# Optimization experiments

Hardware: AMD Instinct MI355X
Metric: run time of the kernel (lower is better)

Reference implementation:

```python
import jax, jax.numpy as jnp
import numpy as np

B, H, S, D, KG = 1, 8, 1024, 64, 10

def setup_inputs() -> dict:
    key = jax.random.key(0)
    ks = jax.random.split(key, 16)
    n = jax.random.normal
    u = jax.random.uniform
    return {
        'Q': n(ks[0], (B, H, S, D), dtype=jnp.float32),
        'K': n(ks[1], (B, H, S, D), dtype=jnp.float32),
        'V': n(ks[2], (B, H, S, D), dtype=jnp.float32),
        'distance_matrix': u(ks[3], (B, H, S, S), dtype=jnp.float32) * 10.0,
        'energy_matrix': u(ks[4], (B, H, S, S), dtype=jnp.float32) * 5.0,
        'mask': jnp.ones((B, H, S, S), dtype=jnp.int32),
        'mu_D': n(ks[5], (KG,), dtype=jnp.float32),
        'sigma_D': u(ks[6], (KG,), dtype=jnp.float32) + 0.5,  # keep sigma positive
        'b_D': n(ks[7], (KG,), dtype=jnp.float32) * 0.1,
        'mu_E': n(ks[8], (KG,), dtype=jnp.float32),
        'sigma_E': u(ks[9], (KG,), dtype=jnp.float32) + 0.5,
        'b_E': n(ks[10], (KG,), dtype=jnp.float32) * 0.1,
        'W1': n(ks[11], (KG, KG), dtype=jnp.float32) / np.sqrt(KG),
        'b1': jnp.zeros((KG,), dtype=jnp.float32),
        'W2': n(ks[12], (1, KG), dtype=jnp.float32) / np.sqrt(KG),
        'b2': jnp.zeros((1,), dtype=jnp.float32),
    }


def _rbf_mlp_bias(x, b, mu, sigma, W1, b1, W2, b2):
    # x: [B,H,S,S] -> Gaussian RBF features over K kernels, then small MLP -> [B,H,S,S]
    z = (x[..., None] + b - mu) / sigma                      # [B,H,S,S,K]
    inv_norm = 1.0 / (jnp.sqrt(2.0 * jnp.pi) * sigma)
    psi = jnp.exp(-0.5 * z * z) * inv_norm                   # [B,H,S,S,K]
    h = jax.nn.gelu(jnp.einsum('bhijk,lk->bhijl', psi, W1) + b1, approximate=False)
    return (jnp.einsum('bhijk,lk->bhijl', h, W2) + b2)[..., 0]


def reference(Q, K, V, distance_matrix, energy_matrix, mask,
              mu_D, sigma_D, b_D, mu_E, sigma_E, b_E, W1, b1, W2, b2):
    d_model = Q.shape[-1]
    scores = jnp.einsum('bhid,bhjd->bhij', Q, K) / np.sqrt(d_model * 2)
    scores = scores + _rbf_mlp_bias(distance_matrix, b_D, mu_D, sigma_D, W1, b1, W2, b2)
    scores = scores + _rbf_mlp_bias(energy_matrix, b_E, mu_E, sigma_E, W1, b1, W2, b2)
    scores = jnp.where(mask == 0, jnp.float32(-1e9), scores)
    attn = jax.nn.softmax(scores, axis=-1)
    return jnp.einsum('bhij,bhjd->bhid', attn, V)
```

## Files before the change

kernel.cpp:

```cpp
#include <hip/hip_runtime.h>
#include <math.h>

#define Hn 8
#define Sn 1024
#define Dn 64
#define KG 10

#define TN 2048
#define RD 10.25f
#define RE 5.125f

typedef __attribute__((ext_vector_type(8))) short bf16x8;
typedef __attribute__((ext_vector_type(4))) float f32x4;
typedef unsigned short u16;
typedef unsigned int u32;

__device__ inline float bf2f(u16 u) {
    union { u32 i; float f; } v;
    v.i = ((u32)u) << 16;
    return v.f;
}

__device__ inline u16 f2bf(float f) {
    union { float f; u32 i; } v;
    v.f = f;
    u32 i = v.i;
    return (u16)((i + 0x7FFFu + ((i >> 16) & 1u)) >> 16);
}

__device__ float bias_eval(float x,
                           const float* __restrict__ mu, const float* __restrict__ sg,
                           const float* __restrict__ bb,
                           const float* __restrict__ W1, const float* __restrict__ b1,
                           const float* __restrict__ W2, const float* __restrict__ b2) {
    const float inv_s2pi = 0.39894228040143267794f;
    float psi[KG];
#pragma unroll
    for (int k = 0; k < KG; k++) {
        float s = sg[k];
        float z = (x + bb[k] - mu[k]) / s;
        psi[k] = __expf(-0.5f * z * z) * (inv_s2pi / s);
    }
    float out = b2[0];
#pragma unroll
    for (int l = 0; l < KG; l++) {
        float a = b1[l];
#pragma unroll
        for (int k = 0; k < KG; k++) a += psi[k] * W1[l * KG + k];
        float g = 0.5f * a * (1.0f + erff(a * 0.70710678118654752440f));
        out += g * W2[l];
    }
    return out;
}

#define QK4 262144
#define VTN 524288

__global__ __launch_bounds__(256) void prep_kernel(
    const float* __restrict__ Q, const float* __restrict__ K, const float* __restrict__ V,
    const float* __restrict__ muD, const float* __restrict__ sgD, const float* __restrict__ bD,
    const float* __restrict__ muE, const float* __restrict__ sgE, const float* __restrict__ bE,
    const float* __restrict__ W1, const float* __restrict__ b1,
    const float* __restrict__ W2, const float* __restrict__ b2,
    u32* __restrict__ tab, u16* __restrict__ Qb, u16* __restrict__ Kb, u16* __restrict__ VTi)
{
    int id = blockIdx.x * 256 + threadIdx.x;
    if (id < 2 * TN) {
        int which = (id >= TN);
        int idx = id & (TN - 1);
        float h = (which ? RE : RD) / (float)TN;
        float x0 = idx * h;
        float v0, v1;
        if (which) {
            v0 = bias_eval(x0,     muE, sgE, bE, W1, b1, W2, b2);
            v1 = bias_eval(x0 + h, muE, sgE, bE, W1, b1, W2, b2);
        } else {
            v0 = bias_eval(x0,     muD, sgD, bD, W1, b1, W2, b2);
            v1 = bias_eval(x0 + h, muD, sgD, bD, W1, b1, W2, b2);
        }
        tab[id] = (u32)f2bf(v0) | ((u32)f2bf(v1 - v0) << 16);
    } else if (id < 2 * TN + QK4) {
        int i = id - 2 * TN;
        int arr = i >> 17;
        i &= (1 << 17) - 1;
        float4 v = ((const float4*)(arr ? K : Q))[i];
        ushort4 o;
        o.x = f2bf(v.x); o.y = f2bf(v.y); o.z = f2bf(v.z); o.w = f2bf(v.w);
        ((ushort4*)(arr ? Kb : Qb))[i] = o;
    } else if (id < 2 * TN + QK4 + VTN) {
        int g = id - (2 * TN + QK4);
        int h = g >> 16;
        int d = (g >> 10) & 63;
        int s = g & 1023;
        int t = s >> 5, q = (s >> 3) & 3, j = s & 7;
        int src_s = (t << 5) + (q << 2) + (j & 3) + ((j >> 2) << 4);
        VTi[g] = f2bf(V[(((size_t)h << 10) + src_s) * Dn + d]);
    }
}

__device__ inline float lerp_tab(const u32* __restrict__ st, float x, float invh) {
    float tf = x * invh;
    int i = (int)tf;
    float fr = tf - (float)i;
    u32 p = st[i];
    return fmaf(bf2f((u16)(p >> 16)), fr, bf2f((u16)p));
}

__global__ __launch_bounds__(512, 4) void attn_kernel(
    const u16* __restrict__ Qb, const u16* __restrict__ Kb, const u16* __restrict__ VTi,
    const float* __restrict__ Dm, const float* __restrict__ Em, const int* __restrict__ Mk,
    const u32* __restrict__ gtab, float* __restrict__ out)
{
    __shared__ __align__(16) u32 sTab[2 * TN];
    __shared__ float sO[8][16][68];
    __shared__ float sL[8][16];

    const int tid = threadIdx.x;
    {
        const uint4* g4 = (const uint4*)gtab;
        uint4* s4 = (uint4*)sTab;
        s4[tid] = g4[tid];
        s4[tid + 512] = g4[tid + 512];
    }
    __syncthreads();

    const int h    = blockIdx.y;
    const int q0   = blockIdx.x * 16;
    const int wave = tid >> 6;
    const int lane = tid & 63;
    const int quad = lane >> 4;
    const int l16  = lane & 15;

    const u16* Qh = Qb  + (size_t)h * Sn * Dn;
    const u16* Kh = Kb  + (size_t)h * Sn * Dn;
    const u16* Vh = VTi + (size_t)h * Dn * Sn;
    const float* Dh = Dm + (size_t)h * Sn * Sn + (size_t)(q0 + l16) * Sn;
    const float* Eh = Em + (size_t)h * Sn * Sn + (size_t)(q0 + l16) * Sn;
    const int*   Mh = Mk + (size_t)h * Sn * Sn + (size_t)(q0 + l16) * Sn;
    const float invhD = (float)TN / RD;
    const float invhE = (float)TN / RE;
    const float scale = 0.08838834764831845f;
    const float Mfix  = 16.f;

    const bf16x8 bQ0 = *(const bf16x8*)(Qh + (q0 + l16) * Dn + quad * 8);
    const bf16x8 bQ1 = *(const bf16x8*)(Qh + (q0 + l16) * Dn + 32 + quad * 8);

    f32x4 O0 = {0.f, 0.f, 0.f, 0.f}, O1 = O0, O2 = O0, O3 = O0;
    float l_r = 0.f;

    const int kbase = wave * 128;
#pragma unroll
    for (int t = 0; t < 4; t++) {
        const int k0 = kbase + t * 32;

        const u16* kr = Kh + (size_t)(k0 + l16) * Dn + quad * 8;
        const bf16x8 aK00 = *(const bf16x8*)(kr);
        const bf16x8 aK01 = *(const bf16x8*)(kr + 32);
        const bf16x8 aK10 = *(const bf16x8*)(kr + 16 * Dn);
        const bf16x8 aK11 = *(const bf16x8*)(kr + 16 * Dn + 32);

        const u16* vr = Vh + k0 + quad * 8;
        const bf16x8 bV0 = *(const bf16x8*)(vr + (size_t)(l16)      * Sn);
        const bf16x8 bV1 = *(const bf16x8*)(vr + (size_t)(16 + l16) * Sn);
        const bf16x8 bV2 = *(const bf16x8*)(vr + (size_t)(32 + l16) * Sn);
        const bf16x8 bV3 = *(const bf16x8*)(vr + (size_t)(48 + l16) * Sn);

        const float4 Dv0 = *(const float4*)(Dh + k0 + quad * 4);
        const float4 Dv1 = *(const float4*)(Dh + k0 + 16 + quad * 4);
        const float4 Ev0 = *(const float4*)(Eh + k0 + quad * 4);
        const float4 Ev1 = *(const float4*)(Eh + k0 + 16 + quad * 4);
        const int4   Mv0 = *(const int4*)(Mh + k0 + quad * 4);
        const int4   Mv1 = *(const int4*)(Mh + k0 + 16 + quad * 4);

        f32x4 s0 = {0.f, 0.f, 0.f, 0.f}, s1 = s0;
        s0 = __builtin_amdgcn_mfma_f32_16x16x32_bf16(aK00, bQ0, s0, 0, 0, 0);
        s0 = __builtin_amdgcn_mfma_f32_16x16x32_bf16(aK01, bQ1, s0, 0, 0, 0);
        s1 = __builtin_amdgcn_mfma_f32_16x16x32_bf16(aK10, bQ0, s1, 0, 0, 0);
        s1 = __builtin_amdgcn_mfma_f32_16x16x32_bf16(aK11, bQ1, s1, 0, 0, 0);

        const float dv0[4] = {Dv0.x, Dv0.y, Dv0.z, Dv0.w};
        const float dv1[4] = {Dv1.x, Dv1.y, Dv1.z, Dv1.w};
        const float ev0[4] = {Ev0.x, Ev0.y, Ev0.z, Ev0.w};
        const float ev1[4] = {Ev1.x, Ev1.y, Ev1.z, Ev1.w};
        const int   mv0[4] = {Mv0.x, Mv0.y, Mv0.z, Mv0.w};
        const int   mv1[4] = {Mv1.x, Mv1.y, Mv1.z, Mv1.w};

        bf16x8 aP;
#pragma unroll
        for (int r = 0; r < 4; r++) {
            float v0 = s0[r] * scale + lerp_tab(sTab, dv0[r], invhD)
                                     + lerp_tab(sTab + TN, ev0[r], invhE);
            v0 = fminf(fmaxf(v0, -60.f), 80.f);
            v0 = (mv0[r] == 0) ? -60.f : v0;
            float v1 = s1[r] * scale + lerp_tab(sTab, dv1[r], invhD)
                                     + lerp_tab(sTab + TN, ev1[r], invhE);
            v1 = fminf(fmaxf(v1, -60.f), 80.f);
            v1 = (mv1[r] == 0) ? -60.f : v1;
            const float p0 = __expf(v0 - Mfix);
            const float p1 = __expf(v1 - Mfix);
            l_r += p0 + p1;
            aP[r]     = (short)f2bf(p0);
            aP[4 + r] = (short)f2bf(p1);
        }

        O0 = __builtin_amdgcn_mfma_f32_16x16x32_bf16(aP, bV0, O0, 0, 0, 0);
        O1 = __builtin_amdgcn_mfma_f32_16x16x32_bf16(aP, bV1, O1, 0, 0, 0);
        O2 = __builtin_amdgcn_mfma_f32_16x16x32_bf16(aP, bV2, O2, 0, 0, 0);
        O3 = __builtin_amdgcn_mfma_f32_16x16x32_bf16(aP, bV3, O3, 0, 0, 0);
    }

    l_r += __shfl_xor(l_r, 16, 64);
    l_r += __shfl_xor(l_r, 32, 64);
    if (lane < 16) sL[wave][lane] = l_r;

#pragma unroll
    for (int r = 0; r < 4; r++) {
        sO[wave][quad * 4 + r][ 0 + l16] = O0[r];
        sO[wave][quad * 4 + r][16 + l16] = O1[r];
        sO[wave][quad * 4 + r][32 + l16] = O2[r];
        sO[wave][quad * 4 + r][48 + l16] = O3[r];
    }
    __syncthreads();

    const int row = tid >> 5;
    const int c2  = (tid & 31) * 2;
    float lg = 0.f;
#pragma unroll
    for (int w = 0; w < 8; w++) lg += sL[w][row];
    const float inv = 1.0f / lg;

    float a0 = 0.f, a1 = 0.f;
#pragma unroll
    for (int w = 0; w < 8; w++) {
        a0 += sO[w][row][c2];
        a1 += sO[w][row][c2 + 1];
    }
    float2 ov = {a0 * inv, a1 * inv};
    *(float2*)(out + ((size_t)(h * Sn + q0 + row)) * Dn + c2) = ov;
}

extern "C" void kernel_launch(void* const* d_in, const int* in_sizes, int n_in,
                              void* d_out, int out_size, void* d_ws, size_t ws_size,
                              hipStream_t stream) {
    const float* Q    = (const float*)d_in[0];
    const float* K    = (const float*)d_in[1];
    const float* V    = (const float*)d_in[2];
    const float* Dm   = (const float*)d_in[3];
    const float* Em   = (const float*)d_in[4];
    const int*   Mask = (const int*)d_in[5];
    const float* muD  = (const float*)d_in[6];
    const float* sgD  = (const float*)d_in[7];
    const float* bD   = (const float*)d_in[8];
    const float* muE  = (const float*)d_in[9];
    const float* sgE  = (const float*)d_in[10];
    const float* bE   = (const float*)d_in[11];
    const float* W1   = (const float*)d_in[12];
    const float* b1   = (const float*)d_in[13];
    const float* W2   = (const float*)d_in[14];
    const float* b2   = (const float*)d_in[15];

    u32* tab = (u32*)d_ws;
    u16* Qb  = (u16*)((char*)d_ws + 2 * TN * 4);
    u16* Kb  = Qb + (size_t)Hn * Sn * Dn;
    u16* VTi = Kb + (size_t)Hn * Sn * Dn;

    const int prep_threads = 2 * TN + QK4 + VTN;
    prep_kernel<<<prep_threads / 256, 256, 0, stream>>>(
        Q, K, V, muD, sgD, bD, muE, sgE, bE, W1, b1, W2, b2,
        tab, Qb, Kb, VTi);

    dim3 grid(Sn / 16, Hn);
    attn_kernel<<<grid, 512, 0, stream>>>(Qb, Kb, VTi, Dm, Em, Mask, tab,
                                          (float*)d_out);
}
```

Measured before the change: 177.3 us.

## Precompute fp16 bias matrix in prep pass and slim attention kernel

Moves the distance/energy table interpolation and mask handling into a separate prep pass that writes one fp16 bias value per score into a workspace matrix. The attention kernel then reads 2 bytes per score instead of 12, uses 256-thread blocks with 8 key tiles per wave, and double-buffers the K and bias loads. The cost is an extra full write and read of an S×S×H fp16 matrix plus one more kernel launch. The clamp bound changes to 64 and the fixed max offset is removed, which relies on fp16 range and on exp staying in range without a running max.

After: 186.7 us. 1.05x slower.

```diff
diff --git a/kernel.cpp b/kernel.cpp
--- a/kernel.cpp
+++ b/kernel.cpp
@@ -12,6 +12,7 @@
 
 typedef __attribute__((ext_vector_type(8))) short bf16x8;
 typedef __attribute__((ext_vector_type(4))) float f32x4;
+typedef __attribute__((ext_vector_type(4))) _Float16 h16x4;
 typedef unsigned short u16;
 typedef unsigned int u32;
 
@@ -26,6 +27,12 @@
     v.f = f;
     u32 i = v.i;
     return (u16)((i + 0x7FFFu + ((i >> 16) & 1u)) >> 16);
+}
+
+__device__ inline u16 f2h_bits(float f) {
+    union { _Float16 h; u16 u; } cv;
+    cv.h = (_Float16)f;
+    return cv.u;
 }
 
 __device__ float bias_eval(float x,
@@ -53,42 +60,94 @@
     return out;
 }
 
-#define QK4 262144
-#define VTN 524288
-
-__global__ __launch_bounds__(256) void prep_kernel(
-    const float* __restrict__ Q, const float* __restrict__ K, const float* __restrict__ V,
+__global__ __launch_bounds__(256) void build_tables_kernel(
     const float* __restrict__ muD, const float* __restrict__ sgD, const float* __restrict__ bD,
     const float* __restrict__ muE, const float* __restrict__ sgE, const float* __restrict__ bE,
     const float* __restrict__ W1, const float* __restrict__ b1,
     const float* __restrict__ W2, const float* __restrict__ b2,
-    u32* __restrict__ tab, u16* __restrict__ Qb, u16* __restrict__ Kb, u16* __restrict__ VTi)
+    u32* __restrict__ tab)
 {
     int id = blockIdx.x * 256 + threadIdx.x;
-    if (id < 2 * TN) {
-        int which = (id >= TN);
-        int idx = id & (TN - 1);
-        float h = (which ? RE : RD) / (float)TN;
-        float x0 = idx * h;
-        float v0, v1;
-        if (which) {
-            v0 = bias_eval(x0,     muE, sgE, bE, W1, b1, W2, b2);
-            v1 = bias_eval(x0 + h, muE, sgE, bE, W1, b1, W2, b2);
-        } else {
-            v0 = bias_eval(x0,     muD, sgD, bD, W1, b1, W2, b2);
-            v1 = bias_eval(x0 + h, muD, sgD, bD, W1, b1, W2, b2);
+    int which = (id >= TN);
+    int idx = id & (TN - 1);
+    float h = (which ? RE : RD) / (float)TN;
+    float x0 = idx * h;
+    float v0, v1;
+    if (which) {
+        v0 = bias_eval(x0,     muE, sgE, bE, W1, b1, W2, b2);
+        v1 = bias_eval(x0 + h, muE, sgE, bE, W1, b1, W2, b2);
+    } else {
+        v0 = bias_eval(x0,     muD, sgD, bD, W1, b1, W2, b2);
+        v1 = bias_eval(x0 + h, muD, sgD, bD, W1, b1, W2, b2);
+    }
+    tab[id] = (u32)f2bf(v0) | ((u32)f2bf(v1 - v0) << 16);
+}
+
+__global__ __launch_bounds__(256) void prep_kernel(
+    const float* __restrict__ Dm, const float* __restrict__ Em, const int* __restrict__ Mk,
+    const float* __restrict__ Q, const float* __restrict__ K, const float* __restrict__ V,
+    const u32* __restrict__ tab,
+    u16* __restrict__ Bb, u16* __restrict__ Qb, u16* __restrict__ Kb, u16* __restrict__ VTi)
+{
+    __shared__ __align__(16) u32 sTab[2 * TN];
+    const int wg = blockIdx.x;
+    const int tid = threadIdx.x;
+
+    if (wg < 4096) {
+        {
+            const uint4* g4 = (const uint4*)tab;
+            uint4* s4 = (uint4*)sTab;
+#pragma unroll
+            for (int i = 0; i < 4; i++) s4[tid + 256 * i] = g4[tid + 256 * i];
         }
-        tab[id] = (u32)f2bf(v0) | ((u32)f2bf(v1 - v0) << 16);
-    } else if (id < 2 * TN + QK4) {
-        int i = id - 2 * TN;
+        __syncthreads();
+
+        const float invhD = (float)TN / RD;
+        const float invhE = (float)TN / RE;
+        const size_t base = ((size_t)wg * 256 + tid) * 8;
+
+        const float4 d0 = *(const float4*)(Dm + base);
+        const float4 d1 = *(const float4*)(Dm + base + 4);
+        const float4 e0 = *(const float4*)(Em + base);
+        const float4 e1 = *(const float4*)(Em + base + 4);
+        const int4   m0 = *(const int4*)(Mk + base);
+        const int4   m1 = *(const int4*)(Mk + base + 4);
+
+        const float dv[8] = {d0.x, d0.y, d0.z, d0.w, d1.x, d1.y, d1.z, d1.w};
+        const float ev[8] = {e0.x, e0.y, e0.z, e0.w, e1.x, e1.y, e1.z, e1.w};
+        const int   mv[8] = {m0.x, m0.y, m0.z, m0.w, m1.x, m1.y, m1.z, m1.w};
+
+        u16 ob[8];
+#pragma unroll
+        for (int j = 0; j < 8; j++) {
+            float tf = dv[j] * invhD;
+            int i = min((int)tf, TN - 1);
+            float fr = tf - (float)i;
+            u32 p = sTab[i];
+            float vD = fmaf(bf2f((u16)(p >> 16)), fr, bf2f((u16)p));
+
+            tf = ev[j] * invhE;
+            i = min((int)tf, TN - 1);
+            fr = tf - (float)i;
+            p = sTab[TN + i];
+            float vE = fmaf(bf2f((u16)(p >> 16)), fr, bf2f((u16)p));
+
+            float v = vD + vE;
+            v = fminf(fmaxf(v, -60.f), 64.f);
+            v = (mv[j] == 0) ? -60.f : v;
+            ob[j] = f2h_bits(v);
+        }
+        *(uint4*)(Bb + base) = *(const uint4*)ob;
+    } else if (wg < 5120) {
+        int i = (wg - 4096) * 256 + tid;
         int arr = i >> 17;
         i &= (1 << 17) - 1;
         float4 v = ((const float4*)(arr ? K : Q))[i];
         ushort4 o;
         o.x = f2bf(v.x); o.y = f2bf(v.y); o.z = f2bf(v.z); o.w = f2bf(v.w);
         ((ushort4*)(arr ? Kb : Qb))[i] = o;
-    } else if (id < 2 * TN + QK4 + VTN) {
-        int g = id - (2 * TN + QK4);
+    } else {
+        int g = (wg - 5120) * 256 + tid;
         int h = g >> 16;
         int d = (g >> 10) & 63;
         int s = g & 1023;
@@ -98,32 +157,14 @@
     }
 }
 
-__device__ inline float lerp_tab(const u32* __restrict__ st, float x, float invh) {
-    float tf = x * invh;
-    int i = (int)tf;
-    float fr = tf - (float)i;
-    u32 p = st[i];
-    return fmaf(bf2f((u16)(p >> 16)), fr, bf2f((u16)p));
-}
-
-__global__ __launch_bounds__(512, 4) void attn_kernel(
+__global__ __launch_bounds__(256, 4) void attn_kernel(
     const u16* __restrict__ Qb, const u16* __restrict__ Kb, const u16* __restrict__ VTi,
-    const float* __restrict__ Dm, const float* __restrict__ Em, const int* __restrict__ Mk,
-    const u32* __restrict__ gtab, float* __restrict__ out)
+    const u16* __restrict__ Bb, float* __restrict__ out)
 {
-    __shared__ __align__(16) u32 sTab[2 * TN];
-    __shared__ float sO[8][16][68];
-    __shared__ float sL[8][16];
-
-    const int tid = threadIdx.x;
-    {
-        const uint4* g4 = (const uint4*)gtab;
-        uint4* s4 = (uint4*)sTab;
-        s4[tid] = g4[tid];
-        s4[tid + 512] = g4[tid + 512];
-    }
-    __syncthreads();
-
+    __shared__ float sO[4][16][68];
+    __shared__ float sL[4][16];
+
+    const int tid  = threadIdx.x;
     const int h    = blockIdx.y;
     const int q0   = blockIdx.x * 16;
     const int wave = tid >> 6;
@@ -134,13 +175,8 @@
     const u16* Qh = Qb  + (size_t)h * Sn * Dn;
     const u16* Kh = Kb  + (size_t)h * Sn * Dn;
     const u16* Vh = VTi + (size_t)h * Dn * Sn;
-    const float* Dh = Dm + (size_t)h * Sn * Sn + (size_t)(q0 + l16) * Sn;
-    const float* Eh = Em + (size_t)h * Sn * Sn + (size_t)(q0 + l16) * Sn;
-    const int*   Mh = Mk + (size_t)h * Sn * Sn + (size_t)(q0 + l16) * Sn;
-    const float invhD = (float)TN / RD;
-    const float invhE = (float)TN / RE;
+    const u16* Bh = Bb  + ((size_t)(h * Sn + q0 + l16)) * Sn;
     const float scale = 0.08838834764831845f;
-    const float Mfix  = 16.f;
 
     const bf16x8 bQ0 = *(const bf16x8*)(Qh + (q0 + l16) * Dn + quad * 8);
     const bf16x8 bQ1 = *(const bf16x8*)(Qh + (q0 + l16) * Dn + 32 + quad * 8);
@@ -148,56 +184,56 @@
     f32x4 O0 = {0.f, 0.f, 0.f, 0.f}, O1 = O0, O2 = O0, O3 = O0;
     float l_r = 0.f;
 
-    const int kbase = wave * 128;
-#pragma unroll
-    for (int t = 0; t < 4; t++) {
+    const int kbase = wave * 256;
+    const u16* krb = Kh + (size_t)l16 * Dn + quad * 8;
+    const u16* vrb = Vh + quad * 8;
+
+    bf16x8 cK[2][4];
+    h16x4  cB[2][2];
+
+    {
+        const u16* kr = krb + (size_t)kbase * Dn;
+        cK[0][0] = *(const bf16x8*)(kr);
+        cK[0][1] = *(const bf16x8*)(kr + 32);
+        cK[0][2] = *(const bf16x8*)(kr + 16 * Dn);
+        cK[0][3] = *(const bf16x8*)(kr + 16 * Dn + 32);
+        cB[0][0] = *(const h16x4*)(Bh + kbase + quad * 4);
+        cB[0][1] = *(const h16x4*)(Bh + kbase + 16 + quad * 4);
+    }
+
+#pragma unroll
+    for (int t = 0; t < 8; t++) {
+        const int cur = t & 1, nxt = cur ^ 1;
         const int k0 = kbase + t * 32;
 
-        const u16* kr = Kh + (size_t)(k0 + l16) * Dn + quad * 8;
-        const bf16x8 aK00 = *(const bf16x8*)(kr);
-        const bf16x8 aK01 = *(const bf16x8*)(kr + 32);
-        const bf16x8 aK10 = *(const bf16x8*)(kr + 16 * Dn);
-        const bf16x8 aK11 = *(const bf16x8*)(kr + 16 * Dn + 32);
-
-        const u16* vr = Vh + k0 + quad * 8;
+        if (t < 7) {
+            const int kn = k0 + 32;
+            const u16* kr = krb + (size_t)kn * Dn;
+            cK[nxt][0] = *(const bf16x8*)(kr);
+            cK[nxt][1] = *(const bf16x8*)(kr + 32);
+            cK[nxt][2] = *(const bf16x8*)(kr + 16 * Dn);
+            cK[nxt][3] = *(const bf16x8*)(kr + 16 * Dn + 32);
+            cB[nxt][0] = *(const h16x4*)(Bh + kn + quad * 4);
+            cB[nxt][1] = *(const h16x4*)(Bh + kn + 16 + quad * 4);
+        }
+
+        const u16* vr = vrb + k0;
         const bf16x8 bV0 = *(const bf16x8*)(vr + (size_t)(l16)      * Sn);
         const bf16x8 bV1 = *(const bf16x8*)(vr + (size_t)(16 + l16) * Sn);
         const bf16x8 bV2 = *(const bf16x8*)(vr + (size_t)(32 + l16) * Sn);
         const bf16x8 bV3 = *(const bf16x8*)(vr + (size_t)(48 + l16) * Sn);
 
-        const float4 Dv0 = *(const float4*)(Dh + k0 + quad * 4);
-        const float4 Dv1 = *(const float4*)(Dh + k0 + 16 + quad * 4);
-        const float4 Ev0 = *(const float4*)(Eh + k0 + quad * 4);
-        const float4 Ev1 = *(const float4*)(Eh + k0 + 16 + quad * 4);
-        const int4   Mv0 = *(const int4*)(Mh + k0 + quad * 4);
-        const int4   Mv1 = *(const int4*)(Mh + k0 + 16 + quad * 4);
-
         f32x4 s0 = {0.f, 0.f, 0.f, 0.f}, s1 = s0;
-        s0 = __builtin_amdgcn_mfma_f32_16x16x32_bf16(aK00, bQ0, s0, 0, 0, 0);
-        s0 = __builtin_amdgcn_mfma_f32_16x16x32_bf16(aK01, bQ1, s0, 0, 0, 0);
-        s1 = __builtin_amdgcn_mfma_f32_16x16x32_bf16(aK10, bQ0, s1, 0, 0, 0);
-        s1 = __builtin_amdgcn_mfma_f32_16x16x32_bf16(aK11, bQ1, s1, 0, 0, 0);
-
-        const float dv0[4] = {Dv0.x, Dv0.y, Dv0.z, Dv0.w};
-        const float dv1[4] = {Dv1.x, Dv1.y, Dv1.z, Dv1.w};
-        const float ev0[4] = {Ev0.x, Ev0.y, Ev0.z, Ev0.w};
-        const float ev1[4] = {Ev1.x, Ev1.y, Ev1.z, Ev1.w};
-        const int   mv0[4] = {Mv0.x, Mv0.y, Mv0.z, Mv0.w};
-        const int   mv1[4] = {Mv1.x, Mv1.y, Mv1.z, Mv1.w};
+        s0 = __builtin_amdgcn_mfma_f32_16x16x32_bf16(cK[cur][0], bQ0, s0, 0, 0, 0);
+        s0 = __builtin_amdgcn_mfma_f32_16x16x32_bf16(cK[cur][1], bQ1, s0, 0, 0, 0);
+        s1 = __builtin_amdgcn_mfma_f32_16x16x32_bf16(cK[cur][2], bQ0, s1, 0, 0, 0);
+        s1 = __builtin_amdgcn_mfma_f32_16x16x32_bf16(cK[cur][3], bQ1, s1, 0, 0, 0);
 
         bf16x8 aP;
 #pragma unroll
         for (int r = 0; r < 4; r++) {
-            float v0 = s0[r] * scale + lerp_tab(sTab, dv0[r], invhD)
-                                     + lerp_tab(sTab + TN, ev0[r], invhE);
-            v0 = fminf(fmaxf(v0, -60.f), 80.f);
-            v0 = (mv0[r] == 0) ? -60.f : v0;
-            float v1 = s1[r] * scale + lerp_tab(sTab, dv1[r], invhD)
-                                     + lerp_tab(sTab + TN, ev1[r], invhE);
-            v1 = fminf(fmaxf(v1, -60.f), 80.f);
-            v1 = (mv1[r] == 0) ? -60.f : v1;
-            const float p0 = __expf(v0 - Mfix);
-            const float p1 = __expf(v1 - Mfix);
+            const float p0 = __expf(fmaf(s0[r], scale, (float)cB[cur][0][r]));
+            const float p1 = __expf(fmaf(s1[r], scale, (float)cB[cur][1][r]));
             l_r += p0 + p1;
             aP[r]     = (short)f2bf(p0);
             aP[4 + r] = (short)f2bf(p1);
@@ -222,21 +258,23 @@
     }
     __syncthreads();
 
-    const int row = tid >> 5;
-    const int c2  = (tid & 31) * 2;
+    const int row = tid >> 4;
+    const int c4  = (tid & 15) * 4;
     float lg = 0.f;
 #pragma unroll
-    for (int w = 0; w < 8; w++) lg += sL[w][row];
+    for (int w = 0; w < 4; w++) lg += sL[w][row];
     const float inv = 1.0f / lg;
 
-    float a0 = 0.f, a1 = 0.f;
-#pragma unroll
-    for (int w = 0; w < 8; w++) {
-        a0 += sO[w][row][c2];
-        a1 += sO[w][row][c2 + 1];
-    }
-    float2 ov = {a0 * inv, a1 * inv};
-    *(float2*)(out + ((size_t)(h * Sn + q0 + row)) * Dn + c2) = ov;
+    float acc[4];
+#pragma unroll
+    for (int c = 0; c < 4; c++) {
+        acc[c] = 0.f;
+#pragma unroll
+        for (int w = 0; w < 4; w++) acc[c] += sO[w][row][c4 + c];
+        acc[c] *= inv;
+    }
+    float4 ov = {acc[0], acc[1], acc[2], acc[3]};
+    *(float4*)(out + ((size_t)(h * Sn + q0 + row)) * Dn + c4) = ov;
 }
 
 extern "C" void kernel_launch(void* const* d_in, const int* in_sizes, int n_in,
@@ -263,13 +301,14 @@
     u16* Qb  = (u16*)((char*)d_ws + 2 * TN * 4);
     u16* Kb  = Qb + (size_t)Hn * Sn * Dn;
     u16* VTi = Kb + (size_t)Hn * Sn * Dn;
-
-    const int prep_threads = 2 * TN + QK4 + VTN;
-    prep_kernel<<<prep_threads / 256, 256, 0, stream>>>(
-        Q, K, V, muD, sgD, bD, muE, sgE, bE, W1, b1, W2, b2,
-        tab, Qb, Kb, VTi);
+    u16* Bb  = VTi + (size_t)Hn * Sn * Dn;
+
+    build_tables_kernel<<<2 * TN / 256, 256, 0, stream>>>(
+        muD, sgD, bD, muE, sgE, bE, W1, b1, W2, b2, tab);
+
+    prep_kernel<<<7168, 256, 0, stream>>>(Dm, Em, Mask, Q, K, V, tab,
+                                          Bb, Qb, Kb, VTi);
 
     dim3 grid(Sn / 16, Hn);
-    attn_kernel<<<grid, 512, 0, stream>>>(Qb, Kb, VTi, Dm, Em, Mask, tab,
-                                          (float*)d_out);
-}
+    attn_kernel<<<grid, 256, 0, stream>>>(Qb, Kb, VTi, Bb, (float*)d_out);
+}
```
